# Optimization experiments

Hardware: AMD Instinct MI355X
Metric: run time of the kernel (lower is better)

The kernel has to match this reference:

```python
import jax, jax.numpy as jnp
import numpy as np


def setup_inputs() -> dict:
    key = jax.random.key(0)
    k1, k2 = jax.random.split(key)
    B, D, H, W = 32, 256, 32, 32
    K = 1024
    z = jax.random.normal(k1, (B, D, H, W), dtype=jnp.float32)
    # torch init is uniform(-1/K, 1/K); randn scaled keeps same scale class
    embedding_weight = jax.random.uniform(k2, (K, D), dtype=jnp.float32,
                                          minval=-1.0 / K, maxval=1.0 / K)
    return {"z": z, "embedding_weight": embedding_weight}


def reference(z, embedding_weight):
    # z: [B, D, H, W] -> [B, H, W, D]
    z_nhwc = jnp.transpose(z, (0, 2, 3, 1))
    B, H, W, D = z_nhwc.shape
    z_flat = z_nhwc.reshape(-1, D)                      # [N, D]
    # squared distances: ||z||^2 + ||e||^2 - 2 z @ e^T   -> [N, K]
    d = (jnp.sum(z_flat ** 2, axis=1, keepdims=True)
         + jnp.sum(embedding_weight ** 2, axis=1)
         - 2.0 * z_flat @ embedding_weight.T)
    min_encoding_indices = jnp.argmin(d, axis=1)        # [N] int
    z_q = embedding_weight[min_encoding_indices].reshape(B, H, W, D)
    memodecode_loss = (jax.lax.stop_gradient(z_q) - z_nhwc) ** 2  # [B,H,W,D]
    z_q_out = jnp.transpose(z_q, (0, 3, 1, 2))          # [B, D, H, W]
    return (z_q_out, min_encoding_indices, memodecode_loss)
```

## Files before the change

### kernel.cpp

```cpp
#include <hip/hip_runtime.h>

#define DD 256
#define HWN 1024
#define NN 32768
#define KK 1024
#define MARGIN 1e-4f
#define FLAGBIT (1 << 30)

#define ZQ_OFF   0
#define IDX_OFF  8388608
#define LOSS_OFF 8421376

#define WS_NEED 38146112

typedef __attribute__((ext_vector_type(8))) _Float16 f16x8;
typedef __attribute__((ext_vector_type(4))) float f32x4;
typedef unsigned long long u64;

__device__ __forceinline__ ushort f2h(float x) {
    _Float16 h = (_Float16)x;
    return *reinterpret_cast<ushort*>(&h);
}
__device__ __forceinline__ float h2f(ushort u) {
    _Float16 h = *reinterpret_cast<_Float16*>(&u);
    return (float)h;
}

__device__ __forceinline__ int swz(int r, int kgi) {
    return (r << 2) + (kgi ^ (r & 3) ^ ((r >> 2) & 3));
}

__global__ __launch_bounds__(256) void k_prepE2(const float* __restrict__ E,
                                                ushort* __restrict__ Eh2,
                                                float* __restrict__ e2,
                                                int* __restrict__ flagCount) {
    __shared__ float ec[32][257];
    const int g = blockIdx.x;
    const int th = threadIdx.x;
    const int n0 = g << 5;
    if (g == 0 && th == 0) *flagCount = 0;
#pragma unroll
    for (int j = 0; j < 32; ++j)
        ec[j][th] = E[(size_t)n0 * DD + (j << 8) + th];
    __syncthreads();
    {
        const int r = th & 31, c = th >> 5;
        const int row = n0 + r;
        const int t = row >> 7, rl = row & 127;
        ushort hs[32];
#pragma unroll
        for (int i = 0; i < 32; ++i)
            hs[i] = f2h(__fmul_rn(ec[r][(c << 5) + i], 1024.f));
        ushort* sb = Eh2 + (size_t)c * 32768 + (size_t)t * 4096;
#pragma unroll
        for (int kgi = 0; kgi < 4; ++kgi)
            *reinterpret_cast<f16x8*>(&sb[swz(rl, kgi) << 3]) =
                *reinterpret_cast<f16x8*>(&hs[kgi << 3]);
    }
    {
        const int row = th >> 3, j = th & 7;
        const float* a = &ec[row][0];
        float x0 = a[j];
        float r0 = __fmul_rn(x0, x0);
        float x1 = a[128 + j];
        float r1 = __fmul_rn(x1, x1);
#pragma unroll
        for (int i = 8; i < 128; i += 8) {
            float y0 = a[i + j];
            r0 = __fadd_rn(r0, __fmul_rn(y0, y0));
            float y1 = a[128 + i + j];
            r1 = __fadd_rn(r1, __fmul_rn(y1, y1));
        }
#pragma unroll
        for (int m = 1; m <= 4; m <<= 1) {
            r0 = __fadd_rn(r0, __shfl_xor(r0, m));
            r1 = __fadd_rn(r1, __shfl_xor(r1, m));
        }
        if (j == 0) e2[n0 + row] = __fadd_rn(r0, r1);
    }
}

__global__ __launch_bounds__(256) void k_prepZ2(const float* __restrict__ Z,
                                                ushort* __restrict__ Zh,
                                                ushort* __restrict__ Zh2,
                                                float* __restrict__ z2) {
    __shared__ float zc[32][257];
    const int g = blockIdx.x;
    const int b = g >> 5;
    const int hw0 = (g & 31) << 5;
    const int th = threadIdx.x;
    const int n0 = (b << 10) + hw0;

#pragma unroll
    for (int j = 0; j < 32; ++j) {
        int li = (j << 8) + th;
        int d = li >> 5;
        int hl = li & 31;
        zc[hl][d] = Z[(size_t)((b << 8) + d) * HWN + hw0 + hl];
    }
    __syncthreads();

    {
        const int r = th & 31, c = th >> 5;
        const int n = n0 + r;
        const int t = n >> 7, rl = n & 127;
        ushort hs[32];
#pragma unroll
        for (int i = 0; i < 32; ++i) hs[i] = f2h(zc[r][(c << 5) + i]);
        size_t addr = (size_t)n * DD + (c << 5);
#pragma unroll
        for (int q = 0; q < 4; ++q)
            *reinterpret_cast<f16x8*>(&Zh[addr + (q << 3)]) =
                *reinterpret_cast<f16x8*>(&hs[q << 3]);
        ushort* sb = Zh2 + (size_t)c * 1048576 + (size_t)t * 4096;
#pragma unroll
        for (int kgi = 0; kgi < 4; ++kgi)
            *reinterpret_cast<f16x8*>(&sb[swz(rl, kgi) << 3]) =
                *reinterpret_cast<f16x8*>(&hs[kgi << 3]);
    }

    {
        const int row = th >> 3, j = th & 7;
        const float* a = &zc[row][0];
        float x0 = a[j];
        float r0 = __fmul_rn(x0, x0);
        float x1 = a[128 + j];
        float r1 = __fmul_rn(x1, x1);
#pragma unroll
        for (int i = 8; i < 128; i += 8) {
            float y0 = a[i + j];
            r0 = __fadd_rn(r0, __fmul_rn(y0, y0));
            float y1 = a[128 + i + j];
            r1 = __fadd_rn(r1, __fmul_rn(y1, y1));
        }
#pragma unroll
        for (int m = 1; m <= 4; m <<= 1) {
            r0 = __fadd_rn(r0, __shfl_xor(r0, m));
            r1 = __fadd_rn(r1, __shfl_xor(r1, m));
        }
        if (j == 0) z2[n0 + row] = __fadd_rn(r0, r1);
    }
}

__global__ __launch_bounds__(256) void k_z2(const float* __restrict__ Z,
                                            float* __restrict__ z2) {
    int n = (blockIdx.x << 8) + threadIdx.x;
    int b = n >> 10, hw = n & 1023;
    const float* base = Z + (size_t)(b << 8) * HWN + hw;
    float half_[2];
#pragma unroll
    for (int h = 0; h < 2; ++h) {
        const float* a = base + (size_t)(h << 7) * HWN;
        float r[8];
#pragma unroll
        for (int j = 0; j < 8; ++j) {
            float x = a[(size_t)j * HWN];
            r[j] = __fmul_rn(x, x);
        }
        for (int i = 8; i < 128; i += 8) {
#pragma unroll
            for (int j = 0; j < 8; ++j) {
                float x = a[(size_t)(i + j) * HWN];
                r[j] = __fadd_rn(r[j], __fmul_rn(x, x));
            }
        }
        half_[h] = __fadd_rn(__fadd_rn(__fadd_rn(r[0], r[1]), __fadd_rn(r[2], r[3])),
                             __fadd_rn(__fadd_rn(r[4], r[5]), __fadd_rn(r[6], r[7])));
    }
    z2[n] = __fadd_rn(half_[0], half_[1]);
}

__device__ __forceinline__ void stage_kc(const ushort* __restrict__ Zs,
                                         const ushort* __restrict__ Es,
                                         ushort* ldsbuf, int zt, int et, int kc,
                                         int wid, int lane) {
#pragma unroll
    for (int is = 0; is < 4; ++is) {
        const int chunk = (wid << 2) + is;
        const int arr = chunk >> 3;
        const int cb8 = chunk & 7;
        const ushort* g = (arr == 0)
            ? Zs + (size_t)kc * 1048576 + (size_t)zt * 4096 + (cb8 << 9) + (lane << 3)
            : Es + (size_t)kc * 32768  + (size_t)et * 4096 + (cb8 << 9) + (lane << 3);
        ushort* l = ldsbuf + arr * 4096 + (cb8 << 9);
        __builtin_amdgcn_global_load_lds(
            (const __attribute__((address_space(1))) void*)g,
            (__attribute__((address_space(3))) void*)l, 16, 0, 0);
    }
}

__global__ __launch_bounds__(256) void k_dist_mfma(const ushort* __restrict__ Zh2,
                                                   const ushort* __restrict__ Eh2,
                                                   const float* __restrict__ e2,
                                                   float* __restrict__ part) {
    __shared__ ushort lds[2][2][4096];
    float (*red)[2][3] = reinterpret_cast<float (*)[2][3]>(&lds[0][0][0]);

    const int B = blockIdx.x;
    const int xcd = B & 7;
    const int j = B >> 3;
    const int cb = j & 7;
    const int rb = (xcd << 5) + (j >> 3);
    const int n0 = rb << 7, c0 = cb << 7;
    const int th = threadIdx.x;
    const int wid = th >> 6, lane = th & 63;
    const int wr = wid >> 1, wc = wid & 1;
    const int fr = lane & 15, kgi = lane >> 4;

    f32x4 acc[4][4];
#pragma unroll
    for (int i = 0; i < 4; ++i)
#pragma unroll
        for (int jj = 0; jj < 4; ++jj) acc[i][jj] = (f32x4){0.f, 0.f, 0.f, 0.f};

    int zoff[4], eoff[4];
#pragma unroll
    for (int mi = 0; mi < 4; ++mi)
        zoff[mi] = swz((wr << 6) + (mi << 4) + fr, kgi) << 4;
#pragma unroll
    for (int ni = 0; ni < 4; ++ni)
        eoff[ni] = swz((wc << 6) + (ni << 4) + fr, kgi) << 4;

    stage_kc(Zh2, Eh2, &lds[0][0][0], rb, cb, 0, wid, lane);

    for (int kc = 0; kc < 8; ++kc) {
        __builtin_amdgcn_s_barrier();
        if (kc < 7) {
            stage_kc(Zh2, Eh2, &lds[(kc + 1) & 1][0][0], rb, cb, kc + 1, wid, lane);
            asm volatile("s_waitcnt vmcnt(4)" ::: "memory");
        } else {
            asm volatile("s_waitcnt vmcnt(0)" ::: "memory");
        }
        __builtin_amdgcn_s_barrier();

        const char* zb  = (const char*)&lds[kc & 1][0][0];
        const char* ebh = (const char*)&lds[kc & 1][1][0];
        f16x8 za[4], ea[4];
#pragma unroll
        for (int mi = 0; mi < 4; ++mi)
            za[mi] = *reinterpret_cast<const f16x8*>(zb + zoff[mi]);
#pragma unroll
        for (int ni = 0; ni < 4; ++ni)
            ea[ni] = *reinterpret_cast<const f16x8*>(ebh + eoff[ni]);
        __builtin_amdgcn_s_setprio(1);
#pragma unroll
        for (int mi = 0; mi < 4; ++mi)
#pragma unroll
            for (int ni = 0; ni < 4; ++ni)
                acc[mi][ni] = __builtin_amdgcn_mfma_f32_16x16x32_f16(za[mi], ea[ni], acc[mi][ni], 0, 0, 0);
        __builtin_amdgcn_s_setprio(0);
    }

    __syncthreads();

    float e2v[4];
#pragma unroll
    for (int ni = 0; ni < 4; ++ni) e2v[ni] = e2[c0 + (wc << 6) + (ni << 4) + fr];

#pragma unroll
    for (int mi = 0; mi < 4; ++mi) {
#pragma unroll
        for (int jj = 0; jj < 4; ++jj) {
            float m1 = __builtin_inff(), m2 = __builtin_inff(), bi = 3.4e38f;
#pragma unroll
            for (int ni = 0; ni < 4; ++ni) {
                float s = fmaf(-0x1p-9f, acc[mi][ni][jj], e2v[ni]);
                float c = (float)(c0 + (wc << 6) + (ni << 4) + fr);
                if (s < m1)      { m2 = m1; m1 = s; bi = c; }
                else if (s < m2) { m2 = s; }
            }
#pragma unroll
            for (int m = 1; m <= 8; m <<= 1) {
                float om1 = __shfl_xor(m1, m);
                float om2 = __shfl_xor(m2, m);
                float obi = __shfl_xor(bi, m);
                if (om1 < m1)       { m2 = fminf(m1, om2); m1 = om1; bi = obi; }
                else if (om1 == m1) { bi = fminf(bi, obi); m2 = m1; }
                else                { m2 = fminf(m2, om1); }
            }
            if (fr == 0) {
                int row = (wr << 6) + (mi << 4) + (kgi << 2) + jj;
                red[row][wc][0] = m1; red[row][wc][1] = m2; red[row][wc][2] = bi;
            }
        }
    }
    __syncthreads();
    if (th < 128) {
        float M1 = red[th][0][0], M2 = red[th][0][1], I = red[th][0][2];
        float v1 = red[th][1][0], v2 = red[th][1][1], vi = red[th][1][2];
        if (v1 < M1)       { M2 = fminf(M1, v2); M1 = v1; I = vi; }
        else if (v1 == M1) { I = fminf(I, vi); M2 = M1; }
        else               { M2 = fminf(M2, v1); }
        size_t p = ((size_t)(n0 + th) * 8 + cb) * 3;
        part[p] = M1; part[p + 1] = M2; part[p + 2] = I;
    }
}

__global__ __launch_bounds__(256) void k_combine(const float* __restrict__ part,
                                                 int* __restrict__ bestIdx,
                                                 int* __restrict__ flagList,
                                                 int* __restrict__ flagCount,
                                                 u64* __restrict__ bestG) {
    int n = (blockIdx.x << 8) + threadIdx.x;
    const float* p = part + (size_t)n * 24;
    float M1 = __builtin_inff(), M2 = __builtin_inff(), I = 3.4e38f;
    for (int c = 0; c < 8; ++c) {
        float v1 = p[c * 3], v2 = p[c * 3 + 1], vi = p[c * 3 + 2];
        if (v1 < M1)       { M2 = fminf(M1, v2); M1 = v1; I = vi; }
        else if (v1 == M1) { I = fminf(I, vi); M2 = M1; }
        else               { M2 = fminf(M2, v1); }
    }
    if (M2 - M1 < MARGIN) {
        bestIdx[n] = (int)I | FLAGBIT;
        bestG[n] = ~0ull;
        int pos = atomicAdd(flagCount, 1);
        flagList[pos] = n;
    } else {
        bestIdx[n] = (int)I;
    }
}

__global__ __launch_bounds__(256) void k_refine5(const float* __restrict__ Z,
                                                 const float* __restrict__ E,
                                                 const float* __restrict__ e2,
                                                 const float* __restrict__ z2,
                                                 const int* __restrict__ flagList,
                                                 const int* __restrict__ flagCount,
                                                 u64* __restrict__ bestG) {
    __shared__ float zsh[4][DD];
    __shared__ float gbv[16][4];
    __shared__ int gbi[16][4];
    __shared__ int rown[4];
    const int th = threadIdx.x;
    const int g = th >> 4;
    const int l = th & 15;
    const int cnt = *flagCount;
    const int items = ((cnt + 3) >> 2) << 2;

    for (int jj = blockIdx.x; jj < items; jj += (int)gridDim.x) {
        const int gi = jj >> 2;
        const int q = jj & 3;
        __syncthreads();
        if (th < 4) {
            int fi = (gi << 2) + th;
            if (fi >= cnt) fi = cnt - 1;
            rown[th] = flagList[fi];
        }
        __syncthreads();
#pragma unroll
        for (int r = 0; r < 4; ++r) {
            int n = rown[r];
            zsh[r][th] = Z[(size_t)(((n >> 10) << 8) + th) * HWN + (n & 1023)];
        }
        __syncthreads();
        float zr[4][16];
#pragma unroll
        for (int r = 0; r < 4; ++r)
#pragma unroll
            for (int jq = 0; jq < 16; ++jq) zr[r][jq] = zsh[r][(l << 4) + jq];
        float z2v[4];
#pragma unroll
        for (int r = 0; r < 4; ++r) z2v[r] = z2[rown[r]];
        float gbest[4];
        int bi[4];
#pragma unroll
        for (int r = 0; r < 4; ++r) { gbest[r] = __builtin_inff(); bi[r] = 0; }

        const int base = q << 8;
        for (int it = 0; it < 4; ++it) {
#pragma unroll
            for (int u = 0; u < 4; ++u) {
                const int c = base + (it << 6) + (u << 4) + g;
                const float* er = &E[(size_t)c * DD + (l << 4)];
                float4 a0 = *reinterpret_cast<const float4*>(er);
                float4 a1 = *reinterpret_cast<const float4*>(er + 4);
                float4 a2 = *reinterpret_cast<const float4*>(er + 8);
                float4 a3 = *reinterpret_cast<const float4*>(er + 12);
                double dots[4];
#pragma unroll
                for (int r = 0; r < 4; ++r) {
                    double s0 = (double)a0.x * zr[r][0]  + (double)a0.y * zr[r][1]
                              + (double)a0.z * zr[r][2]  + (double)a0.w * zr[r][3];
                    double s1 = (double)a1.x * zr[r][4]  + (double)a1.y * zr[r][5]
                              + (double)a1.z * zr[r][6]  + (double)a1.w * zr[r][7];
                    double s2 = (double)a2.x * zr[r][8]  + (double)a2.y * zr[r][9]
                              + (double)a2.z * zr[r][10] + (double)a2.w * zr[r][11];
                    double s3 = (double)a3.x * zr[r][12] + (double)a3.y * zr[r][13]
                              + (double)a3.z * zr[r][14] + (double)a3.w * zr[r][15];
                    dots[r] = (s0 + s1) + (s2 + s3);
                }
#pragma unroll
                for (int m = 1; m <= 8; m <<= 1) {
#pragma unroll
                    for (int r = 0; r < 4; ++r)
                        dots[r] += __shfl_xor(dots[r], m);
                }
                if (l == 0) {
#pragma unroll
                    for (int r = 0; r < 4; ++r) {
                        float cc = (float)dots[r];
                        float t2 = __fmul_rn(2.0f, cc);
                        float gg = __fsub_rn(__fadd_rn(z2v[r], e2[c]), t2);
                        if (gg < gbest[r]) { gbest[r] = gg; bi[r] = c; }
                    }
                }
            }
        }
        if (l == 0) {
#pragma unroll
            for (int r = 0; r < 4; ++r) { gbv[g][r] = gbest[r]; gbi[g][r] = bi[r]; }
        }
        __syncthreads();
        if (th < 4) {
            const int r = th;
            float best = gbv[0][r]; int bbi = gbi[0][r];
            for (int qq = 1; qq < 16; ++qq) {
                float v = gbv[qq][r]; int vi = gbi[qq][r];
                if (v < best || (v == best && vi < bbi)) { best = v; bbi = vi; }
            }
            u64 pack = ((u64)__float_as_uint(best) << 32) | (unsigned)bbi;
            atomicMin(&bestG[rown[r]], pack);
        }
    }
}

#define UPD(m1, m2, i1, s, k)                            \
    do {                                                 \
        if ((s) < (m1)) { m2 = m1; m1 = (s); i1 = (k); } \
        else if ((s) < (m2)) { m2 = (s); }               \
    } while (0)

#define FMAJ(j, EV, C)                                   \
    acc[0][j] = fmaf(z4.x, EV.C, acc[0][j]);             \
    acc[1][j] = fmaf(z4.y, EV.C, acc[1][j]);             \
    acc[2][j] = fmaf(z4.z, EV.C, acc[2][j]);             \
    acc[3][j] = fmaf(z4.w, EV.C, acc[3][j]);

#define UROUND(u, C)                                                          \
    {                                                                         \
        float4 z4 = *reinterpret_cast<const float4*>(&zs[dq + u][ty4]);       \
        FMAJ(0, e0, C) FMAJ(1, e1, C) FMAJ(2, e2v, C) FMAJ(3, e3, C)          \
        FMAJ(4, e4, C) FMAJ(5, e5, C) FMAJ(6, e6, C) FMAJ(7, e7, C)           \
    }

__global__ __launch_bounds__(256, 3) void k_dist_f32(const float* __restrict__ Z,
                                                     const float* __restrict__ E,
                                                     const float* __restrict__ e2,
                                                     int* __restrict__ bestIdx) {
    __shared__ float zs[64][68];
    __shared__ float es[128][68];
    const int th = threadIdx.x;
    const int n0 = blockIdx.x << 6;
    const int b = n0 >> 10;
    const int hw0 = n0 & 1023;
    const int tx = th & 15;
    const int ty = th >> 4;
    const int ty4 = ty << 2;
    float m1[4], m2[4];
    int idx[4];
#pragma unroll
    for (int i = 0; i < 4; ++i) { m1[i] = __builtin_inff(); m2[i] = __builtin_inff(); idx[i] = 0; }
    for (int ct = 0; ct < 8; ++ct) {
        float acc[4][8];
#pragma unroll
        for (int i = 0; i < 4; ++i)
#pragma unroll
            for (int j = 0; j < 8; ++j) acc[i][j] = 0.f;
        for (int dc = 0; dc < 4; ++dc) {
            __syncthreads();
#pragma unroll
            for (int j = 0; j < 4; ++j) {
                int i4 = (j << 8) + th;
                int dd = i4 >> 4;
                int rr = (i4 & 15) << 2;
                *reinterpret_cast<float4*>(&zs[dd][rr]) =
                    *reinterpret_cast<const float4*>(
                        &Z[(size_t)((b << 8) + (dc << 6) + dd) * HWN + hw0 + rr]);
            }
#pragma unroll
            for (int j = 0; j < 8; ++j) {
                int i4 = (j << 8) + th;
                int c = i4 >> 4;
                int d4 = (i4 & 15) << 2;
                *reinterpret_cast<float4*>(&es[c][d4]) =
                    *reinterpret_cast<const float4*>(
                        &E[(size_t)((ct << 7) + c) * DD + (dc << 6) + d4]);
            }
            __syncthreads();
#pragma unroll
            for (int dq = 0; dq < 64; dq += 4) {
                float4 e0 = *reinterpret_cast<const float4*>(&es[tx][dq]);
                float4 e1 = *reinterpret_cast<const float4*>(&es[tx + 16][dq]);
                float4 e2v = *reinterpret_cast<const float4*>(&es[tx + 32][dq]);
                float4 e3 = *reinterpret_cast<const float4*>(&es[tx + 48][dq]);
                float4 e4 = *reinterpret_cast<const float4*>(&es[tx + 64][dq]);
                float4 e5 = *reinterpret_cast<const float4*>(&es[tx + 80][dq]);
                float4 e6 = *reinterpret_cast<const float4*>(&es[tx + 96][dq]);
                float4 e7 = *reinterpret_cast<const float4*>(&es[tx + 112][dq]);
                UROUND(0, x)
                UROUND(1, y)
                UROUND(2, z)
                UROUND(3, w)
            }
        }
#pragma unroll
        for (int j = 0; j < 8; ++j) {
            int c = (ct << 7) + tx + (j << 4);
            float en = e2[c];
#pragma unroll
            for (int i = 0; i < 4; ++i) {
                float s = fmaf(-2.f, acc[i][j], en);
                UPD(m1[i], m2[i], idx[i], s, c);
            }
        }
    }
    __syncthreads();
    float* red = &es[0][0];
#pragma unroll
    for (int i = 0; i < 4; ++i) {
        int r = ty4 + i;
        int base = ((r << 4) + tx) * 3;
        red[base] = m1[i]; red[base + 1] = m2[i]; red[base + 2] = (float)idx[i];
    }
    __syncthreads();
    if (th < 64) {
        float M1 = __builtin_inff(), M2 = __builtin_inff(), I = 3.4e38f;
        for (int t = 0; t < 16; ++t) {
            int base = ((th << 4) + t) * 3;
            float v1 = red[base], v2 = red[base + 1], vi = red[base + 2];
            if (v1 < M1)       { M2 = fminf(M1, v2); M1 = v1; I = vi; }
            else if (v1 == M1) { I = fminf(I, vi); M2 = fminf(M2, v1); M2 = fminf(M2, v2); }
            else               { M2 = fminf(M2, v1); }
        }
        int id = (int)I;
        bestIdx[n0 + th] = (M2 - M1 < MARGIN) ? (id | FLAGBIT) : id;
    }
}

__global__ __launch_bounds__(64) void k_refine(const float* __restrict__ Z,
                                               const float* __restrict__ E,
                                               const float* __restrict__ e2,
                                               const float* __restrict__ z2,
                                               int* __restrict__ bestIdx) {
    __shared__ float zr[DD];
    const int l = threadIdx.x;
    for (int i = 0; i < 16; ++i) {
        int n = (blockIdx.x << 4) + i;
        if (!(bestIdx[n] & FLAGBIT)) continue;
        int b = n >> 10, hw = n & 1023;
        __syncthreads();
#pragma unroll
        for (int j = 0; j < 4; ++j)
            zr[(l << 2) + j] = Z[(size_t)((b << 8) + (l << 2) + j) * HWN + hw];
        __syncthreads();
        const float z2v = z2[n];
        float gbest = __builtin_inff();
        int bi = KK;
        for (int kk = 0; kk < 16; ++kk) {
            int k = (kk << 6) + l;
            double dot = 0.0;
            for (int d = 0; d < DD; d += 4) {
                float4 e4 = *reinterpret_cast<const float4*>(&E[(size_t)k * DD + d]);
                dot += (double)e4.x * zr[d]     + (double)e4.y * zr[d + 1]
                     + (double)e4.z * zr[d + 2] + (double)e4.w * zr[d + 3];
            }
            float c = (float)dot;
            float t = __fmul_rn(2.0f, c);
            float gg = __fsub_rn(__fadd_rn(z2v, e2[k]), t);
            if (gg < gbest) { gbest = gg; bi = k; }
        }
#pragma unroll
        for (int off = 32; off > 0; off >>= 1) {
            float og = __shfl_down(gbest, off);
            int oi = __shfl_down(bi, off);
            if (og < gbest || (og == gbest && oi < bi)) { gbest = og; bi = oi; }
        }
        if (l == 0) bestIdx[n] = bi;
    }
}

__global__ __launch_bounds__(256) void k_out(const ushort* __restrict__ Zh,
                                             const float* __restrict__ E,
                                             const int* __restrict__ bestIdx,
                                             const u64* __restrict__ bestG,
                                             float* __restrict__ out) {
    __shared__ int idxs[64];
    __shared__ float es[64][68];
    const int th = threadIdx.x;
    const int n0 = blockIdx.x << 6;
    const int b = n0 >> 10;
    const int hw0 = n0 & 1023;

    if (th < 64) {
        int n = n0 + th;
        int v = bestIdx[n];
        int id = (v & FLAGBIT) ? (int)(unsigned)(bestG[n] & 1023ull) : (v & 1023);
        idxs[th] = id;
        out[IDX_OFF + n] = (float)id;
    }
    __syncthreads();

#pragma unroll
    for (int j = 0; j < 16; ++j) {
        int i4 = (j << 8) + th;
        int r = i4 >> 6;
        int f = (i4 & 63) << 2;
        int n = n0 + r;
        float4 e4 = *reinterpret_cast<const float4*>(&E[(size_t)idxs[r] * DD + f]);
        ushort4 zu = *reinterpret_cast<const ushort4*>(&Zh[(size_t)n * DD + f]);
        float4 o;
        float t;
        t = e4.x - h2f(zu.x); o.x = t * t;
        t = e4.y - h2f(zu.y); o.y = t * t;
        t = e4.z - h2f(zu.z); o.z = t * t;
        t = e4.w - h2f(zu.w); o.w = t * t;
        *reinterpret_cast<float4*>(&out[LOSS_OFF + (size_t)n * DD + f]) = o;
    }

    for (int dc = 0; dc < 4; ++dc) {
        __syncthreads();
        {
            const int r = th >> 2, qd = (th & 3) << 4;
            const float* er = &E[(size_t)idxs[r] * DD + (dc << 6) + qd];
#pragma unroll
            for (int v = 0; v < 4; ++v)
                *reinterpret_cast<float4*>(&es[r][qd + (v << 2)]) =
                    *reinterpret_cast<const float4*>(er + (v << 2));
        }
        __syncthreads();
#pragma unroll
        for (int j = 0; j < 16; ++j) {
            int li = (j << 8) + th;
            int dd = li >> 6;
            int r = li & 63;
            out[ZQ_OFF + (size_t)((b << 8) + (dc << 6) + dd) * HWN + hw0 + r] =
                es[r][dd];
        }
    }
}

__global__ __launch_bounds__(256) void k_out_f32(const float* __restrict__ Z,
                                                 const float* __restrict__ E,
                                                 const int* __restrict__ bestIdx,
                                                 float* __restrict__ out) {
    __shared__ float zc[64][68];
    __shared__ int idxs[64];
    const int th = threadIdx.x;
    const int n0 = blockIdx.x << 6;
    const int b = n0 >> 10;
    const int hw0 = n0 & 1023;

    if (th < 64) {
        int id = bestIdx[n0 + th] & 1023;
        idxs[th] = id;
        out[IDX_OFF + n0 + th] = (float)id;
    }
    __syncthreads();

    for (int dc = 0; dc < 4; ++dc) {
        __syncthreads();
#pragma unroll
        for (int j = 0; j < 16; ++j) {
            int li = (j << 8) + th;
            int dd = li >> 6;
            int r = li & 63;
            zc[r][dd] = Z[(size_t)((b << 8) + (dc << 6) + dd) * HWN + hw0 + r];
        }
        __syncthreads();
#pragma unroll
        for (int j = 0; j < 4; ++j) {
            int i4 = (j << 8) + th;
            int r = i4 >> 4;
            int f = (i4 & 15) << 2;
            float4 e4 = *reinterpret_cast<const float4*>(
                &E[(size_t)idxs[r] * DD + (dc << 6) + f]);
            float4 z4 = *reinterpret_cast<const float4*>(&zc[r][f]);
            float4 o;
            o.x = (e4.x - z4.x) * (e4.x - z4.x);
            o.y = (e4.y - z4.y) * (e4.y - z4.y);
            o.z = (e4.z - z4.z) * (e4.z - z4.z);
            o.w = (e4.w - z4.w) * (e4.w - z4.w);
            *reinterpret_cast<float4*>(
                &out[LOSS_OFF + (size_t)(n0 + r) * DD + (dc << 6) + f]) = o;
        }
#pragma unroll
        for (int j = 0; j < 16; ++j) {
            int li = (j << 8) + th;
            int dd = li >> 6;
            int r = li & 63;
            out[ZQ_OFF + (size_t)((b << 8) + (dc << 6) + dd) * HWN + hw0 + r] =
                E[(size_t)idxs[r] * DD + (dc << 6) + dd];
        }
    }
}

extern "C" void kernel_launch(void* const* d_in, const int* in_sizes, int n_in,
                              void* d_out, int out_size, void* d_ws, size_t ws_size,
                              hipStream_t stream) {
    const float* Z = (const float*)d_in[0];
    const float* E = (const float*)d_in[1];
    float* out = (float*)d_out;
    char* ws = (char*)d_ws;
    float* e2 = (float*)ws;
    float* z2 = (float*)(ws + 4096);
    int* bestIdx = (int*)(ws + 135168);

    if (ws_size >= WS_NEED) {
        float* part = (float*)(ws + 266240);
        ushort* Eh2 = (ushort*)(ws + 3411968);
        ushort* Zh = (ushort*)(ws + 3936256);
        ushort* Zh2 = (ushort*)(ws + 20713472);
        u64* bestG = (u64*)(ws + 37490688);
        int* flagCount = (int*)(ws + 37752832);
        int* flagList = (int*)(ws + 37752896);
        k_prepE2<<<32, 256, 0, stream>>>(E, Eh2, e2, flagCount);
        k_prepZ2<<<1024, 256, 0, stream>>>(Z, Zh, Zh2, z2);
        k_dist_mfma<<<2048, 256, 0, stream>>>(Zh2, Eh2, e2, part);
        k_combine<<<NN / 256, 256, 0, stream>>>(part, bestIdx, flagList, flagCount, bestG);
        k_refine5<<<2048, 256, 0, stream>>>(Z, E, e2, z2, flagList, flagCount, bestG);
        k_out<<<NN / 64, 256, 0, stream>>>(Zh, E, bestIdx, bestG, out);
    } else {
        k_z2<<<NN / 256, 256, 0, stream>>>(Z, z2);
        k_prepE2<<<32, 256, 0, stream>>>(E, (ushort*)(ws + 266240), e2, (int*)(ws + 266240 + 524288));
        k_dist_f32<<<NN / 64, 256, 0, stream>>>(Z, E, e2, bestIdx);
        k_refine<<<NN / 16, 64, 0, stream>>>(Z, E, e2, z2, bestIdx);
        k_out_f32<<<NN / 64, 256, 0, stream>>>(Z, E, bestIdx, out);
    }
}
```

Before: 143.3 us.

## Widen MFMA distance tile to 128x256 codes per block

The distance kernel's block tile grows from 128 codes to 256 codes, so each staged Z chunk is reused across twice as many codebook columns. The grid is halved, Z reloads from global memory drop by half, and each wave now issues 32 MFMAs per k-chunk instead of 16. The partial-min buffer and combine kernel are resized to 4 column blocks. In exchange, accumulator registers double and LDS use grows, which may cut occupancy. With fewer blocks, the GPU may also be less evenly filled.

Measured after the change: 163.3 us. 1.14x slower.

```diff
diff --git a/kernel.cpp b/kernel.cpp
--- a/kernel.cpp
+++ b/kernel.cpp
@@ -172,17 +172,22 @@
 
 __device__ __forceinline__ void stage_kc(const ushort* __restrict__ Zs,
                                          const ushort* __restrict__ Es,
-                                         ushort* ldsbuf, int zt, int et, int kc,
+                                         ushort* ldsbuf, int rb, int cb, int kc,
                                          int wid, int lane) {
 #pragma unroll
-    for (int is = 0; is < 4; ++is) {
-        const int chunk = (wid << 2) + is;
-        const int arr = chunk >> 3;
-        const int cb8 = chunk & 7;
-        const ushort* g = (arr == 0)
-            ? Zs + (size_t)kc * 1048576 + (size_t)zt * 4096 + (cb8 << 9) + (lane << 3)
-            : Es + (size_t)kc * 32768  + (size_t)et * 4096 + (cb8 << 9) + (lane << 3);
-        ushort* l = ldsbuf + arr * 4096 + (cb8 << 9);
+    for (int is = 0; is < 6; ++is) {
+        const int chunk = wid * 6 + is;
+        const ushort* g;
+        ushort* l;
+        if (chunk < 8) {
+            g = Zs + (size_t)kc * 1048576 + (size_t)rb * 4096 + (chunk << 9) + (lane << 3);
+            l = ldsbuf + (chunk << 9);
+        } else {
+            const int ce = chunk - 8;
+            const int et = (cb << 1) + (ce >> 3);
+            g = Es + (size_t)kc * 32768 + (size_t)et * 4096 + ((ce & 7) << 9) + (lane << 3);
+            l = ldsbuf + 4096 + (ce << 9);
+        }
         __builtin_amdgcn_global_load_lds(
             (const __attribute__((address_space(1))) void*)g,
             (__attribute__((address_space(3))) void*)l, 16, 0, 0);
@@ -193,69 +198,70 @@
                                                    const ushort* __restrict__ Eh2,
                                                    const float* __restrict__ e2,
                                                    float* __restrict__ part) {
-    __shared__ ushort lds[2][2][4096];
-    float (*red)[2][3] = reinterpret_cast<float (*)[2][3]>(&lds[0][0][0]);
+    __shared__ ushort lds[2][12288];
+    float (*red)[2][3] = reinterpret_cast<float (*)[2][3]>(&lds[0][0]);
 
     const int B = blockIdx.x;
     const int xcd = B & 7;
     const int j = B >> 3;
-    const int cb = j & 7;
-    const int rb = (xcd << 5) + (j >> 3);
-    const int n0 = rb << 7, c0 = cb << 7;
+    const int cb = j & 3;
+    const int rb = (xcd << 5) + (j >> 2);
+    const int n0 = rb << 7, c0 = cb << 8;
     const int th = threadIdx.x;
     const int wid = th >> 6, lane = th & 63;
     const int wr = wid >> 1, wc = wid & 1;
     const int fr = lane & 15, kgi = lane >> 4;
 
-    f32x4 acc[4][4];
+    f32x4 acc[4][8];
 #pragma unroll
     for (int i = 0; i < 4; ++i)
 #pragma unroll
-        for (int jj = 0; jj < 4; ++jj) acc[i][jj] = (f32x4){0.f, 0.f, 0.f, 0.f};
-
-    int zoff[4], eoff[4];
+        for (int jj = 0; jj < 8; ++jj) acc[i][jj] = (f32x4){0.f, 0.f, 0.f, 0.f};
+
+    int zoff[4], eoff[8];
 #pragma unroll
     for (int mi = 0; mi < 4; ++mi)
         zoff[mi] = swz((wr << 6) + (mi << 4) + fr, kgi) << 4;
 #pragma unroll
-    for (int ni = 0; ni < 4; ++ni)
-        eoff[ni] = swz((wc << 6) + (ni << 4) + fr, kgi) << 4;
-
-    stage_kc(Zh2, Eh2, &lds[0][0][0], rb, cb, 0, wid, lane);
+    for (int ni = 0; ni < 8; ++ni) {
+        int code = (wc << 7) + (ni << 4) + fr;
+        eoff[ni] = (8192 + ((code >> 7) << 13)) + (swz(code & 127, kgi) << 4);
+    }
+
+    stage_kc(Zh2, Eh2, &lds[0][0], rb, cb, 0, wid, lane);
 
     for (int kc = 0; kc < 8; ++kc) {
         __builtin_amdgcn_s_barrier();
         if (kc < 7) {
-            stage_kc(Zh2, Eh2, &lds[(kc + 1) & 1][0][0], rb, cb, kc + 1, wid, lane);
-            asm volatile("s_waitcnt vmcnt(4)" ::: "memory");
+            stage_kc(Zh2, Eh2, &lds[(kc + 1) & 1][0], rb, cb, kc + 1, wid, lane);
+            asm volatile("s_waitcnt vmcnt(6)" ::: "memory");
         } else {
             asm volatile("s_waitcnt vmcnt(0)" ::: "memory");
         }
         __builtin_amdgcn_s_barrier();
 
-        const char* zb  = (const char*)&lds[kc & 1][0][0];
-        const char* ebh = (const char*)&lds[kc & 1][1][0];
-        f16x8 za[4], ea[4];
+        const char* bb = (const char*)&lds[kc & 1][0];
+        f16x8 za[4], ea[8];
 #pragma unroll
         for (int mi = 0; mi < 4; ++mi)
-            za[mi] = *reinterpret_cast<const f16x8*>(zb + zoff[mi]);
-#pragma unroll
-        for (int ni = 0; ni < 4; ++ni)
-            ea[ni] = *reinterpret_cast<const f16x8*>(ebh + eoff[ni]);
+            za[mi] = *reinterpret_cast<const f16x8*>(bb + zoff[mi]);
+#pragma unroll
+        for (int ni = 0; ni < 8; ++ni)
+            ea[ni] = *reinterpret_cast<const f16x8*>(bb + eoff[ni]);
         __builtin_amdgcn_s_setprio(1);
 #pragma unroll
         for (int mi = 0; mi < 4; ++mi)
 #pragma unroll
-            for (int ni = 0; ni < 4; ++ni)
+            for (int ni = 0; ni < 8; ++ni)
                 acc[mi][ni] = __builtin_amdgcn_mfma_f32_16x16x32_f16(za[mi], ea[ni], acc[mi][ni], 0, 0, 0);
         __builtin_amdgcn_s_setprio(0);
     }
 
     __syncthreads();
 
-    float e2v[4];
-#pragma unroll
-    for (int ni = 0; ni < 4; ++ni) e2v[ni] = e2[c0 + (wc << 6) + (ni << 4) + fr];
+    float e2v[8];
+#pragma unroll
+    for (int ni = 0; ni < 8; ++ni) e2v[ni] = e2[c0 + (wc << 7) + (ni << 4) + fr];
 
 #pragma unroll
     for (int mi = 0; mi < 4; ++mi) {
@@ -263,9 +269,9 @@
         for (int jj = 0; jj < 4; ++jj) {
             float m1 = __builtin_inff(), m2 = __builtin_inff(), bi = 3.4e38f;
 #pragma unroll
-            for (int ni = 0; ni < 4; ++ni) {
+            for (int ni = 0; ni < 8; ++ni) {
                 float s = fmaf(-0x1p-9f, acc[mi][ni][jj], e2v[ni]);
-                float c = (float)(c0 + (wc << 6) + (ni << 4) + fr);
+                float c = (float)(c0 + (wc << 7) + (ni << 4) + fr);
                 if (s < m1)      { m2 = m1; m1 = s; bi = c; }
                 else if (s < m2) { m2 = s; }
             }
@@ -291,7 +297,7 @@
         if (v1 < M1)       { M2 = fminf(M1, v2); M1 = v1; I = vi; }
         else if (v1 == M1) { I = fminf(I, vi); M2 = M1; }
         else               { M2 = fminf(M2, v1); }
-        size_t p = ((size_t)(n0 + th) * 8 + cb) * 3;
+        size_t p = ((size_t)(n0 + th) * 4 + cb) * 3;
         part[p] = M1; part[p + 1] = M2; part[p + 2] = I;
     }
 }
@@ -302,9 +308,9 @@
                                                  int* __restrict__ flagCount,
                                                  u64* __restrict__ bestG) {
     int n = (blockIdx.x << 8) + threadIdx.x;
-    const float* p = part + (size_t)n * 24;
+    const float* p = part + (size_t)n * 12;
     float M1 = __builtin_inff(), M2 = __builtin_inff(), I = 3.4e38f;
-    for (int c = 0; c < 8; ++c) {
+    for (int c = 0; c < 4; ++c) {
         float v1 = p[c * 3], v2 = p[c * 3 + 1], vi = p[c * 3 + 2];
         if (v1 < M1)       { M2 = fminf(M1, v2); M1 = v1; I = vi; }
         else if (v1 == M1) { I = fminf(I, vi); M2 = M1; }
@@ -715,7 +721,7 @@
         int* flagList = (int*)(ws + 37752896);
         k_prepE2<<<32, 256, 0, stream>>>(E, Eh2, e2, flagCount);
         k_prepZ2<<<1024, 256, 0, stream>>>(Z, Zh, Zh2, z2);
-        k_dist_mfma<<<2048, 256, 0, stream>>>(Zh2, Eh2, e2, part);
+        k_dist_mfma<<<1024, 256, 0, stream>>>(Zh2, Eh2, e2, part);
         k_combine<<<NN / 256, 256, 0, stream>>>(part, bestIdx, flagList, flagCount, bestG);
         k_refine5<<<2048, 256, 0, stream>>>(Z, E, e2, z2, flagList, flagCount, bestG);
         k_out<<<NN / 64, 256, 0, stream>>>(Zh, E, bestIdx, bestG, out);
```
